# Performance work log

Measured on AMD Instinct MI355X. Metric: run time of the kernel, lower is better.

## Reference

```python
import jax, jax.numpy as jnp
import numpy as np

N = 50000      # num_nodes
R = 8          # num_relations
FIN = 128      # in_channels
H = 128        # hidden_channels
E = 800000     # num_edges (avg degree 16)


def _xavier(key, shape):
    fan_in, fan_out = shape[-2], shape[-1]
    lim = np.sqrt(6.0 / (fan_in + fan_out)).astype(np.float32)
    return jax.random.uniform(key, shape, jnp.float32, -lim, lim)


def setup_inputs() -> dict:
    key = jax.random.key(0)
    ks = jax.random.split(key, 10)
    return {
        "x": jax.random.normal(ks[0], (N, FIN), jnp.float32),
        "edge_index": jax.random.randint(ks[1], (2, E), 0, N, jnp.int32),
        "edge_type": jax.random.randint(ks[2], (E,), 0, R, jnp.int32),
        "rel_w0": _xavier(ks[3], (R, FIN, H)),
        "root_w0": _xavier(ks[4], (FIN, H)),
        "bias0": jnp.zeros((H,), jnp.float32),
        "rel_w1": _xavier(ks[5], (R, H, H)),
        "root_w1": _xavier(ks[6], (H, H)),
        "bias1": jnp.zeros((H,), jnp.float32),
        "rel_emb": _xavier(ks[7], (R, H)),
    }


def _rgcn_conv(x, src, dst, etype, rel_w, root_w, bias):
    # RGCNConv (PyG, aggr='mean'): out_i = root(x_i) + sum_r W_r * mean_{j in N_r(i)} x_j
    n = x.shape[0]
    seg = dst * R + etype                                   # fused (node, relation) segment id
    msgs = x[src]                                           # [E, F] gather
    sums = jax.ops.segment_sum(msgs, seg, num_segments=n * R)
    cnt = jax.ops.segment_sum(jnp.ones((src.shape[0], 1), x.dtype), seg, num_segments=n * R)
    mean = (sums / jnp.maximum(cnt, 1.0)).reshape(n, R, -1)  # [N, R, F]
    return jnp.einsum('nrf,rfh->nh', mean, rel_w) + x @ root_w + bias


def reference(x, edge_index, edge_type, rel_w0, root_w0, bias0,
              rel_w1, root_w1, bias1, rel_emb):
    src, dst = edge_index[0], edge_index[1]
    h = _rgcn_conv(x, src, dst, edge_type, rel_w0, root_w0, bias0)
    h = jax.nn.relu(h)  # dropout in eval mode (identity)
    h = _rgcn_conv(h, src, dst, edge_type, rel_w1, root_w1, bias1)
    return (h, rel_emb)
```

## Files before the change

kernel.cpp:

```cpp
#include <hip/hip_runtime.h>

typedef unsigned short ushort_t;
typedef __attribute__((ext_vector_type(8))) short short8;
typedef __attribute__((ext_vector_type(4))) float f32x4;
typedef __attribute__((ext_vector_type(4))) int int4v;

#define RNUM 8
#define FDIM 128
#define KDIM 1152

__device__ __forceinline__ float bf2f(ushort_t u) {
    union { unsigned int i; float f; } x;
    x.i = ((unsigned int)u) << 16;
    return x.f;
}
__device__ __forceinline__ ushort_t f2bf(float f) {
    union { float f; unsigned int i; } x;
    x.f = f;
    unsigned int u = x.i;
    u += 0x7fffu + ((u >> 16) & 1u);
    return (ushort_t)(u >> 16);
}

__device__ __forceinline__ void gl_lds16(const void* g, void* s) {
    __builtin_amdgcn_global_load_lds(
        (const __attribute__((address_space(1))) unsigned int*)g,
        (__attribute__((address_space(3))) unsigned int*)s, 16, 0, 0);
}


__global__ void init_head(int* __restrict__ head, int n) {
    int i = blockIdx.x * 256 + threadIdx.x;
    if (i < n) head[i] = -1;
}

__global__ void link_kernel(const int* __restrict__ dst, const int* __restrict__ et,
                            int* head, int* __restrict__ nxt, int E) {
    int i = blockIdx.x * 256 + threadIdx.x;
    if (i < E) {
        int seg = dst[i] * RNUM + et[i];
        nxt[i] = atomicExch(&head[seg], i);
    }
}


__global__ __launch_bounds__(256) void transpose_w(const float* __restrict__ rel_w,
                                                   const float* __restrict__ root_w,
                                                   ushort_t* __restrict__ Wt) {
    int r = blockIdx.x;
    const float* src = (r < 8) ? (rel_w + r * 16384) : root_w;
    __shared__ ushort_t t[128 * 130];
    for (int idx = threadIdx.x; idx < 16384; idx += 256)
        t[(idx >> 7) * 130 + (idx & 127)] = f2bf(src[idx]);
    __syncthreads();
    ushort_t* d = Wt + r * 16384;
    for (int idx = threadIdx.x; idx < 16384; idx += 256)
        d[idx] = t[(idx & 127) * 130 + (idx >> 7)];
}


__global__ void cast_x(const float* __restrict__ x, ushort_t* __restrict__ Mx, int total) {
    int i = (blockIdx.x * 256 + threadIdx.x) * 8;
    if (i >= total) return;
    float4 v0 = *(const float4*)(x + i);
    float4 v1 = *(const float4*)(x + i + 4);
    ushort_t o[8] = {f2bf(v0.x), f2bf(v0.y), f2bf(v0.z), f2bf(v0.w),
                     f2bf(v1.x), f2bf(v1.y), f2bf(v1.z), f2bf(v1.w)};
    int row = i >> 7, col = i & 127;
    *(int4v*)(Mx + (size_t)row * KDIM + 1024 + col) = *(int4v*)o;
}


__global__ __launch_bounds__(256) void seg_mean(const int* __restrict__ head,
                                                const int* __restrict__ nxt,
                                                const int* __restrict__ esrc,
                                                ushort_t* Mx, int NSEG) {
    int t = blockIdx.x * 256 + threadIdx.x;
    int seg = t >> 4;
    int l16 = t & 15;
    if (seg >= NSEG) return;
    float acc[8];
#pragma unroll
    for (int k = 0; k < 8; ++k) acc[k] = 0.f;
    const ushort_t* gbase = Mx + 1024 + (size_t)l16 * 8;
    int cnt = 0;
    int j = head[seg];
    while (j >= 0) {
        int s = esrc[j];
        int jn = nxt[j];
        int4v v = *(const int4v*)(gbase + (size_t)s * KDIM);
        ushort_t* p = (ushort_t*)&v;
#pragma unroll
        for (int k = 0; k < 8; ++k) acc[k] += bf2f(p[k]);
        ++cnt;
        j = jn;
    }
    float sc = (cnt > 0) ? 1.0f / (float)cnt : 0.f;
    ushort_t ov[8];
#pragma unroll
    for (int k = 0; k < 8; ++k) ov[k] = f2bf(acc[k] * sc);
    *(int4v*)(Mx + (size_t)(seg >> 3) * KDIM + (seg & 7) * 128 + l16 * 8) = *(int4v*)ov;
}


template <bool FINAL>
__global__ __launch_bounds__(256) void rgcn_gemm(
    const ushort_t* Mx, const ushort_t* __restrict__ Wt,
    const float* __restrict__ bias, float* __restrict__ outF,
    ushort_t* MxOut, int N) {
    __shared__ ushort_t As[128 * 128];
    __shared__ ushort_t Bs[128 * 128];
    int tid = threadIdx.x;
    int wid = tid >> 6, lane = tid & 63;
    int l16 = lane & 15, q = lane >> 4;
    int nodeBase = blockIdx.x * 128;

    f32x4 acc[2][8];
#pragma unroll
    for (int rt = 0; rt < 2; ++rt)
#pragma unroll
        for (int ct = 0; ct < 8; ++ct) acc[rt][ct] = (f32x4){0.f, 0.f, 0.f, 0.f};

    for (int r = 0; r < 9; ++r) {
        __syncthreads();
#pragma unroll
        for (int i = 0; i < 8; ++i) {
            int L = i * 256 + tid;
            int row = L >> 4;
            int c = (L & 15) ^ (row & 15);
            gl_lds16(Mx + (size_t)(nodeBase + row) * KDIM + r * 128 + c * 8,
                     (char*)As + (size_t)L * 16);
            gl_lds16(Wt + r * 16384 + row * 128 + c * 8,
                     (char*)Bs + (size_t)L * 16);
        }
        __syncthreads();
#pragma unroll
        for (int s = 0; s < 4; ++s) {
            int pos = ((s * 4 + q) ^ l16) * 16;
            short8 a0 = *(const short8*)((const char*)As + ((2 * wid + 0) * 16 + l16) * 256 + pos);
            short8 a1 = *(const short8*)((const char*)As + ((2 * wid + 1) * 16 + l16) * 256 + pos);
#pragma unroll
            for (int ct = 0; ct < 8; ++ct) {
                short8 b = *(const short8*)((const char*)Bs + (ct * 16 + l16) * 256 + pos);
                acc[0][ct] = __builtin_amdgcn_mfma_f32_16x16x32_bf16(a0, b, acc[0][ct], 0, 0, 0);
                acc[1][ct] = __builtin_amdgcn_mfma_f32_16x16x32_bf16(a1, b, acc[1][ct], 0, 0, 0);
            }
        }
    }
#pragma unroll
    for (int rt = 0; rt < 2; ++rt) {
#pragma unroll
        for (int ct = 0; ct < 8; ++ct) {
            int h = ct * 16 + l16;
            float bv = bias[h];
#pragma unroll
            for (int reg = 0; reg < 4; ++reg) {
                int node = nodeBase + (2 * wid + rt) * 16 + q * 4 + reg;
                if (node < N) {
                    float v = acc[rt][ct][reg] + bv;
                    if (FINAL) {
                        outF[(size_t)node * FDIM + h] = v;
                    } else {
                        v = fmaxf(v, 0.f);
                        MxOut[(size_t)node * KDIM + 1024 + h] = f2bf(v);
                    }
                }
            }
        }
    }
}

__global__ void copy_emb(const float* __restrict__ e, float* __restrict__ out, int n) {
    int i = blockIdx.x * 256 + threadIdx.x;
    if (i < n) out[i] = e[i];
}


extern "C" void kernel_launch(void* const* d_in, const int* in_sizes, int n_in,
                              void* d_out, int out_size, void* d_ws, size_t ws_size,
                              hipStream_t stream) {
    const float* x        = (const float*)d_in[0];
    const int* edge_index = (const int*)d_in[1];
    const int* edge_type  = (const int*)d_in[2];
    const float* rel_w0   = (const float*)d_in[3];
    const float* root_w0  = (const float*)d_in[4];
    const float* bias0    = (const float*)d_in[5];
    const float* rel_w1   = (const float*)d_in[6];
    const float* root_w1  = (const float*)d_in[7];
    const float* bias1    = (const float*)d_in[8];
    const float* rel_emb  = (const float*)d_in[9];

    int N = in_sizes[0] / FDIM;
    int E = in_sizes[1] / 2;
    int NSEG = N * RNUM;
    const int* src = edge_index;
    const int* dst = edge_index + E;

    int nb_gemm = (N + 127) / 128;
    int NPAD = nb_gemm * 128;

    char* w = (char*)d_ws;
    auto alloc = [&](size_t bytes) -> char* {
        char* p = w;
        w += (bytes + 255) & ~(size_t)255;
        return p;
    };
    int* head    = (int*)alloc((size_t)NSEG * 4);
    int* nxt     = (int*)alloc((size_t)E * 4);
    ushort_t* Wt = (ushort_t*)alloc((size_t)2 * 9 * 16384 * 2);
    ushort_t* Mx = (ushort_t*)alloc((size_t)NPAD * KDIM * 2);
    (void)ws_size; (void)n_in; (void)out_size;

    int nb_seg  = (NSEG + 255) / 256;
    int nb_E    = (E + 255) / 256;
    int nb_mean = (NSEG * 16) / 256;
    int nb_cast = (N * FDIM) / (256 * 8);

    init_head<<<nb_seg, 256, 0, stream>>>(head, NSEG);
    link_kernel<<<nb_E, 256, 0, stream>>>(dst, edge_type, head, nxt, E);
    transpose_w<<<9, 256, 0, stream>>>(rel_w0, root_w0, Wt);
    transpose_w<<<9, 256, 0, stream>>>(rel_w1, root_w1, Wt + 9 * 16384);
    cast_x<<<nb_cast, 256, 0, stream>>>(x, Mx, N * FDIM);

    seg_mean<<<nb_mean, 256, 0, stream>>>(head, nxt, src, Mx, NSEG);
    rgcn_gemm<false><<<nb_gemm, 256, 0, stream>>>(Mx, Wt, bias0, nullptr, Mx, N);
    seg_mean<<<nb_mean, 256, 0, stream>>>(head, nxt, src, Mx, NSEG);
    rgcn_gemm<true><<<nb_gemm, 256, 0, stream>>>(Mx, Wt + 9 * 16384, bias1,
                                                 (float*)d_out, nullptr, N);
    copy_emb<<<4, 256, 0, stream>>>(rel_emb, (float*)d_out + (size_t)N * FDIM,
                                    in_sizes[9]);
}
```

Measured before the change: 333.3 us.

## Fuse segment-mean aggregation into the RGCN GEMM kernel per relation

Replaces the separate seg_mean pass and the wide [N,1152] intermediate with a fused kernel. For each relation, 1024 threads walk the linked edge lists of a 128-node tile, write the bf16 means straight into LDS, and then run MFMA against that relation's weight slice. This removes the global write and re-read of the aggregated matrix and two launches. The gather loop now splits its accumulation across two accumulators to shorten dependency chains, and head init becomes a memset. The cost is that the irregular gather latency now sits inside the GEMM block with no overlap across relations, and the larger blocks with more LDS may lower occupancy.

```diff
diff --git a/kernel.cpp b/kernel.cpp
--- a/kernel.cpp
+++ b/kernel.cpp
@@ -7,7 +7,6 @@
 
 #define RNUM 8
 #define FDIM 128
-#define KDIM 1152
 
 __device__ __forceinline__ float bf2f(ushort_t u) {
     union { unsigned int i; float f; } x;
@@ -28,11 +27,6 @@
         (__attribute__((address_space(3))) unsigned int*)s, 16, 0, 0);
 }
 
-
-__global__ void init_head(int* __restrict__ head, int n) {
-    int i = blockIdx.x * 256 + threadIdx.x;
-    if (i < n) head[i] = -1;
-}
 
 __global__ void link_kernel(const int* __restrict__ dst, const int* __restrict__ et,
                             int* head, int* __restrict__ nxt, int E) {
@@ -59,111 +53,122 @@
 }
 
 
-__global__ void cast_x(const float* __restrict__ x, ushort_t* __restrict__ Mx, int total) {
+__global__ void cast_x(const float* __restrict__ x, ushort_t* __restrict__ o, int total) {
     int i = (blockIdx.x * 256 + threadIdx.x) * 8;
     if (i >= total) return;
-    float4 v0 = *(const float4*)(x + i);
-    float4 v1 = *(const float4*)(x + i + 4);
-    ushort_t o[8] = {f2bf(v0.x), f2bf(v0.y), f2bf(v0.z), f2bf(v0.w),
-                     f2bf(v1.x), f2bf(v1.y), f2bf(v1.z), f2bf(v1.w)};
-    int row = i >> 7, col = i & 127;
-    *(int4v*)(Mx + (size_t)row * KDIM + 1024 + col) = *(int4v*)o;
-}
-
-
-__global__ __launch_bounds__(256) void seg_mean(const int* __restrict__ head,
-                                                const int* __restrict__ nxt,
-                                                const int* __restrict__ esrc,
-                                                ushort_t* Mx, int NSEG) {
-    int t = blockIdx.x * 256 + threadIdx.x;
-    int seg = t >> 4;
-    int l16 = t & 15;
-    if (seg >= NSEG) return;
-    float acc[8];
-#pragma unroll
-    for (int k = 0; k < 8; ++k) acc[k] = 0.f;
-    const ushort_t* gbase = Mx + 1024 + (size_t)l16 * 8;
-    int cnt = 0;
-    int j = head[seg];
-    while (j >= 0) {
-        int s = esrc[j];
-        int jn = nxt[j];
-        int4v v = *(const int4v*)(gbase + (size_t)s * KDIM);
-        ushort_t* p = (ushort_t*)&v;
-#pragma unroll
-        for (int k = 0; k < 8; ++k) acc[k] += bf2f(p[k]);
-        ++cnt;
-        j = jn;
-    }
-    float sc = (cnt > 0) ? 1.0f / (float)cnt : 0.f;
-    ushort_t ov[8];
-#pragma unroll
-    for (int k = 0; k < 8; ++k) ov[k] = f2bf(acc[k] * sc);
-    *(int4v*)(Mx + (size_t)(seg >> 3) * KDIM + (seg & 7) * 128 + l16 * 8) = *(int4v*)ov;
+    float4 a = *(const float4*)(x + i);
+    float4 b = *(const float4*)(x + i + 4);
+    ushort_t t[8] = {f2bf(a.x), f2bf(a.y), f2bf(a.z), f2bf(a.w),
+                     f2bf(b.x), f2bf(b.y), f2bf(b.z), f2bf(b.w)};
+    *(int4v*)(o + i) = *(int4v*)t;
 }
 
 
 template <bool FINAL>
-__global__ __launch_bounds__(256) void rgcn_gemm(
-    const ushort_t* Mx, const ushort_t* __restrict__ Wt,
-    const float* __restrict__ bias, float* __restrict__ outF,
-    ushort_t* MxOut, int N) {
+__global__ __launch_bounds__(1024) void fused_conv(
+    const ushort_t* __restrict__ Xg,
+    const int* __restrict__ head,
+    const int* __restrict__ nxt, const int* __restrict__ esrc,
+    const ushort_t* __restrict__ Wt,
+    const float* __restrict__ bias,
+    float* __restrict__ outF, ushort_t* __restrict__ outBf, int N) {
     __shared__ ushort_t As[128 * 128];
     __shared__ ushort_t Bs[128 * 128];
+    __shared__ int headS[1024];
+    __shared__ float biasS[128];
     int tid = threadIdx.x;
     int wid = tid >> 6, lane = tid & 63;
     int l16 = lane & 15, q = lane >> 4;
+    int qw = tid >> 4;
     int nodeBase = blockIdx.x * 128;
 
-    f32x4 acc[2][8];
-#pragma unroll
-    for (int rt = 0; rt < 2; ++rt)
-#pragma unroll
-        for (int ct = 0; ct < 8; ++ct) acc[rt][ct] = (f32x4){0.f, 0.f, 0.f, 0.f};
+    headS[tid] = head[nodeBase * RNUM + tid];
+    if (tid < 128) biasS[tid] = bias[tid];
+
+    f32x4 acc[4];
+#pragma unroll
+    for (int ct = 0; ct < 4; ++ct) acc[ct] = (f32x4){0.f, 0.f, 0.f, 0.f};
+
+    const ushort_t* gbase = Xg + (size_t)l16 * 8;
 
     for (int r = 0; r < 9; ++r) {
         __syncthreads();
 #pragma unroll
-        for (int i = 0; i < 8; ++i) {
-            int L = i * 256 + tid;
+        for (int i = 0; i < 2; ++i) {
+            int L = i * 1024 + tid;
             int row = L >> 4;
             int c = (L & 15) ^ (row & 15);
-            gl_lds16(Mx + (size_t)(nodeBase + row) * KDIM + r * 128 + c * 8,
-                     (char*)As + (size_t)L * 16);
-            gl_lds16(Wt + r * 16384 + row * 128 + c * 8,
-                     (char*)Bs + (size_t)L * 16);
+            gl_lds16(Wt + r * 16384 + row * 128 + c * 8, (char*)Bs + (size_t)L * 16);
+        }
+        if (r == 8) {
+#pragma unroll
+            for (int i = 0; i < 2; ++i) {
+                int L = i * 1024 + tid;
+                int row = L >> 4;
+                int c = (L & 15) ^ (row & 15);
+                gl_lds16(Xg + (size_t)(nodeBase + row) * FDIM + c * 8,
+                         (char*)As + (size_t)L * 16);
+            }
+        } else {
+#pragma unroll
+            for (int g = 0; g < 2; ++g) {
+                int nl = qw * 2 + g;
+                float acc0[8], acc1[8];
+#pragma unroll
+                for (int k = 0; k < 8; ++k) { acc0[k] = 0.f; acc1[k] = 0.f; }
+                int cnt = 0;
+                int j = headS[nl * RNUM + r];
+                while (j >= 0) {
+                    int s = esrc[j];
+                    int jn = nxt[j];
+                    int4v v = *(const int4v*)(gbase + (size_t)s * FDIM);
+                    ushort_t* p = (ushort_t*)&v;
+                    if (cnt & 1) {
+#pragma unroll
+                        for (int k = 0; k < 8; ++k) acc1[k] += bf2f(p[k]);
+                    } else {
+#pragma unroll
+                        for (int k = 0; k < 8; ++k) acc0[k] += bf2f(p[k]);
+                    }
+                    ++cnt;
+                    j = jn;
+                }
+                float sc = (cnt > 0) ? 1.0f / (float)cnt : 0.f;
+                ushort_t ov[8];
+#pragma unroll
+                for (int k = 0; k < 8; ++k) ov[k] = f2bf((acc0[k] + acc1[k]) * sc);
+                *(int4v*)((char*)As + nl * 256 + ((l16 ^ (nl & 15)) * 16)) = *(int4v*)ov;
+            }
         }
         __syncthreads();
+        int rw = wid & 7, ch = wid >> 3;
 #pragma unroll
         for (int s = 0; s < 4; ++s) {
-            int pos = ((s * 4 + q) ^ l16) * 16;
-            short8 a0 = *(const short8*)((const char*)As + ((2 * wid + 0) * 16 + l16) * 256 + pos);
-            short8 a1 = *(const short8*)((const char*)As + ((2 * wid + 1) * 16 + l16) * 256 + pos);
-#pragma unroll
-            for (int ct = 0; ct < 8; ++ct) {
-                short8 b = *(const short8*)((const char*)Bs + (ct * 16 + l16) * 256 + pos);
-                acc[0][ct] = __builtin_amdgcn_mfma_f32_16x16x32_bf16(a0, b, acc[0][ct], 0, 0, 0);
-                acc[1][ct] = __builtin_amdgcn_mfma_f32_16x16x32_bf16(a1, b, acc[1][ct], 0, 0, 0);
+            short8 a = *(const short8*)((const char*)As +
+                        (rw * 16 + l16) * 256 + (((s * 4 + q) ^ l16) * 16));
+#pragma unroll
+            for (int ct = 0; ct < 4; ++ct) {
+                int h = ch * 64 + ct * 16 + l16;
+                short8 b = *(const short8*)((const char*)Bs +
+                            h * 256 + (((s * 4 + q) ^ (h & 15)) * 16));
+                acc[ct] = __builtin_amdgcn_mfma_f32_16x16x32_bf16(a, b, acc[ct], 0, 0, 0);
             }
         }
     }
-#pragma unroll
-    for (int rt = 0; rt < 2; ++rt) {
-#pragma unroll
-        for (int ct = 0; ct < 8; ++ct) {
-            int h = ct * 16 + l16;
-            float bv = bias[h];
-#pragma unroll
-            for (int reg = 0; reg < 4; ++reg) {
-                int node = nodeBase + (2 * wid + rt) * 16 + q * 4 + reg;
-                if (node < N) {
-                    float v = acc[rt][ct][reg] + bv;
-                    if (FINAL) {
-                        outF[(size_t)node * FDIM + h] = v;
-                    } else {
-                        v = fmaxf(v, 0.f);
-                        MxOut[(size_t)node * KDIM + 1024 + h] = f2bf(v);
-                    }
+    int rw = wid & 7, ch = wid >> 3;
+#pragma unroll
+    for (int ct = 0; ct < 4; ++ct) {
+        int h = ch * 64 + ct * 16 + l16;
+        float bv = biasS[h];
+#pragma unroll
+        for (int reg = 0; reg < 4; ++reg) {
+            int node = nodeBase + rw * 16 + q * 4 + reg;
+            if (node < N) {
+                float v = acc[ct][reg] + bv;
+                if (FINAL) {
+                    outF[(size_t)node * FDIM + h] = v;
+                } else {
+                    outBf[(size_t)node * FDIM + h] = f2bf(fmaxf(v, 0.f));
                 }
             }
         }
@@ -192,12 +197,11 @@
 
     int N = in_sizes[0] / FDIM;
     int E = in_sizes[1] / 2;
-    int NSEG = N * RNUM;
     const int* src = edge_index;
     const int* dst = edge_index + E;
 
-    int nb_gemm = (N + 127) / 128;
-    int NPAD = nb_gemm * 128;
+    int nb_conv = (N + 127) / 128;
+    int NPAD = nb_conv * 128;
 
     char* w = (char*)d_ws;
     auto alloc = [&](size_t bytes) -> char* {
@@ -205,28 +209,27 @@
         w += (bytes + 255) & ~(size_t)255;
         return p;
     };
-    int* head    = (int*)alloc((size_t)NSEG * 4);
-    int* nxt     = (int*)alloc((size_t)E * 4);
-    ushort_t* Wt = (ushort_t*)alloc((size_t)2 * 9 * 16384 * 2);
-    ushort_t* Mx = (ushort_t*)alloc((size_t)NPAD * KDIM * 2);
+    int* head      = (int*)alloc((size_t)NPAD * RNUM * 4);
+    int* nxt       = (int*)alloc((size_t)E * 4);
+    ushort_t* Wt   = (ushort_t*)alloc((size_t)2 * 9 * 16384 * 2);
+    ushort_t* Xbf  = (ushort_t*)alloc((size_t)NPAD * FDIM * 2);
+    ushort_t* hbuf = (ushort_t*)alloc((size_t)NPAD * FDIM * 2);
     (void)ws_size; (void)n_in; (void)out_size;
 
-    int nb_seg  = (NSEG + 255) / 256;
     int nb_E    = (E + 255) / 256;
-    int nb_mean = (NSEG * 16) / 256;
     int nb_cast = (N * FDIM) / (256 * 8);
 
-    init_head<<<nb_seg, 256, 0, stream>>>(head, NSEG);
+    hipMemsetAsync(head, 0xFF, (size_t)NPAD * RNUM * 4, stream);
     link_kernel<<<nb_E, 256, 0, stream>>>(dst, edge_type, head, nxt, E);
     transpose_w<<<9, 256, 0, stream>>>(rel_w0, root_w0, Wt);
     transpose_w<<<9, 256, 0, stream>>>(rel_w1, root_w1, Wt + 9 * 16384);
-    cast_x<<<nb_cast, 256, 0, stream>>>(x, Mx, N * FDIM);
-
-    seg_mean<<<nb_mean, 256, 0, stream>>>(head, nxt, src, Mx, NSEG);
-    rgcn_gemm<false><<<nb_gemm, 256, 0, stream>>>(Mx, Wt, bias0, nullptr, Mx, N);
-    seg_mean<<<nb_mean, 256, 0, stream>>>(head, nxt, src, Mx, NSEG);
-    rgcn_gemm<true><<<nb_gemm, 256, 0, stream>>>(Mx, Wt + 9 * 16384, bias1,
-                                                 (float*)d_out, nullptr, N);
+    cast_x<<<nb_cast, 256, 0, stream>>>(x, Xbf, N * FDIM);
+
+    fused_conv<false><<<nb_conv, 1024, 0, stream>>>(Xbf, head, nxt, src, Wt, bias0,
+                                                    nullptr, hbuf, N);
+    fused_conv<true><<<nb_conv, 1024, 0, stream>>>(hbuf, head, nxt, src,
+                                                   Wt + 9 * 16384, bias1,
+                                                   (float*)d_out, nullptr, N);
     copy_emb<<<4, 256, 0, stream>>>(rel_emb, (float*)d_out + (size_t)N * FDIM,
                                     in_sizes[9]);
 }
```

Measured after the change: 429.0 us. 28.7% more time.
